# Kernel tuning notes

Measured on AMD Instinct MI355X. Metric: run time of the kernel, lower is better.

## Reference

```python
import jax, jax.numpy as jnp
import numpy as np

B, T, C = 2, 2048, 2048
NH, NKV = 16, 4
HD = C // NH  # 128


def setup_inputs() -> dict:
    key = jax.random.key(0)
    ks = jax.random.split(key, 5)
    w = lambda k, shape: jax.random.normal(k, shape, jnp.float32) * 0.02
    return {
        "x": jax.random.normal(ks[0], (B, T, C), jnp.float32),
        "Wq": w(ks[1], (C, C)),
        "Wk": w(ks[2], (C, NKV * HD)),
        "Wv": w(ks[3], (C, NKV * HD)),
        "Wproj": w(ks[4], (C, C)),
    }


def _rope(x):
    # x: [B, H, T, D]; rotate-half RoPE with base 10000
    D = x.shape[-1]
    t = x.shape[-2]
    inv_freq = 1.0 / (10000.0 ** (jnp.arange(0, D, 2, dtype=jnp.float32) / D))
    freqs = jnp.arange(t, dtype=jnp.float32)[:, None] * inv_freq[None, :]  # [T, D/2]
    emb = jnp.concatenate([freqs, freqs], axis=-1)  # [T, D]
    cos, sin = jnp.cos(emb), jnp.sin(emb)
    x1, x2 = x[..., : D // 2], x[..., D // 2 :]
    rotated = jnp.concatenate([-x2, x1], axis=-1)
    return x * cos + rotated * sin


def reference(x, Wq, Wk, Wv, Wproj):
    b, t, c = x.shape
    q = (x @ Wq).reshape(b, t, NH, HD).transpose(0, 2, 1, 3)    # [B,NH,T,HD]
    k = (x @ Wk).reshape(b, t, NKV, HD).transpose(0, 2, 1, 3)   # [B,NKV,T,HD]
    v = (x @ Wv).reshape(b, t, NKV, HD).transpose(0, 2, 1, 3)
    q = _rope(q)
    k = _rope(k)
    rep = NH // NKV
    k = jnp.repeat(k, rep, axis=1)  # [B,NH,T,HD]
    v = jnp.repeat(v, rep, axis=1)
    scale = 1.0 / jnp.sqrt(jnp.float32(HD))
    scores = jnp.einsum("bhqd,bhkd->bhqk", q, k) * scale        # [B,NH,T,T]
    causal = jnp.tril(jnp.ones((t, t), dtype=bool))
    scores = jnp.where(causal, scores, jnp.finfo(scores.dtype).min)
    attn = jax.nn.softmax(scores, axis=-1)
    y = jnp.einsum("bhqk,bhkd->bhqd", attn, v)                  # [B,NH,T,HD]
    y = y.transpose(0, 2, 1, 3).reshape(b, t, c)
    return y @ Wproj
```

## Files before the change

### kernel.cpp

```cpp
#include <hip/hip_runtime.h>

#define B_ 2
#define T_ 2048
#define C_ 2048
#define NH_ 16
#define NKV_ 4
#define HD_ 128
#define M_ 4096
#define NQKV_ 3072

typedef __bf16 bf16x8 __attribute__((ext_vector_type(8)));
typedef float f32x4 __attribute__((ext_vector_type(4)));
typedef float f32x16 __attribute__((ext_vector_type(16)));

__device__ __forceinline__ unsigned short f2bf(float f) {
  union { float f; unsigned u; } c{f};
  unsigned u = c.u + 0x7FFFu + ((c.u >> 16) & 1u);
  return (unsigned short)(u >> 16);
}
__device__ __forceinline__ float bf2f(unsigned short h) {
  union { unsigned u; float f; } c{(unsigned)h << 16};
  return c.f;
}

#define GLOAD_LDS16(g, l)                                        \
  __builtin_amdgcn_global_load_lds(                              \
      (const __attribute__((address_space(1))) void*)(g),        \
      (__attribute__((address_space(3))) void*)(l), 16, 0, 0)

__global__ void rope_table_kernel(float2* __restrict__ rt) {
  int t = blockIdx.x, i = threadIdx.x;
  float inv = powf(10000.f, -(float)(2 * i) / 128.f);
  float s, c;
  sincosf((float)t * inv, &s, &c);
  rt[t * 64 + i] = make_float2(c, s);
}

__global__ void convx_kernel(const float* __restrict__ x, unsigned short* __restrict__ xb, int n4) {
  int i = blockIdx.x * blockDim.x + threadIdx.x;
  if (i >= n4) return;
  float4 v = reinterpret_cast<const float4*>(x)[i];
  union { ushort4 u; unsigned short s[4]; } o;
  o.s[0] = f2bf(v.x); o.s[1] = f2bf(v.y); o.s[2] = f2bf(v.z); o.s[3] = f2bf(v.w);
  reinterpret_cast<ushort4*>(xb)[i] = o.u;
}

__global__ void transpose_conv4_kernel(const float* __restrict__ Wq, const float* __restrict__ Wk,
                                       const float* __restrict__ Wv, const float* __restrict__ Wp,
                                       unsigned short* __restrict__ wt) {
  __shared__ float tile[32][33];
  int id = blockIdx.x;
  const float* W;
  unsigned short* Wt;
  int N, bx, by;
  if (id < 4096)      { W = Wq; Wt = wt;                          N = 2048; int u = id;        bx = u & 63; by = u >> 6; }
  else if (id < 5120) { W = Wk; Wt = wt + (size_t)2048 * 2048;    N = 512;  int u = id - 4096; bx = u & 15; by = u >> 4; }
  else if (id < 6144) { W = Wv; Wt = wt + (size_t)2560 * 2048;    N = 512;  int u = id - 5120; bx = u & 15; by = u >> 4; }
  else                { W = Wp; Wt = wt + (size_t)3072 * 2048;    N = 2048; int u = id - 6144; bx = u & 63; by = u >> 6; }
  const int K = 2048;
  bx *= 32; by *= 32;
  int tx = threadIdx.x & 31, ty = threadIdx.x >> 5;
#pragma unroll
  for (int r = 0; r < 32; r += 8)
    tile[ty + r][tx] = W[(size_t)(by + ty + r) * N + bx + tx];
  __syncthreads();
#pragma unroll
  for (int r = 0; r < 32; r += 8)
    Wt[(size_t)(bx + ty + r) * K + by + tx] = f2bf(tile[tx][ty + r]);
}

__global__ void transpose_v_kernel(const unsigned short* __restrict__ qkv,
                                   unsigned short* __restrict__ vt2) {
  __shared__ unsigned short tile[64][136];
  int bt = blockIdx.x;
  int bh = bt >> 5, t = bt & 31;
  int b = bh >> 2, kvh = bh & 3;
  int tid = threadIdx.x;
#pragma unroll
  for (int p = 0; p < 4; ++p) {
    int kv = p * 16 + (tid >> 4);
    int c8 = (tid & 15) * 8;
    *reinterpret_cast<uint4*>(&tile[kv][c8]) = *reinterpret_cast<const uint4*>(
        &qkv[(size_t)(b * T_ + t * 64 + kv) * NQKV_ + 2560 + kvh * HD_ + c8]);
  }
  __syncthreads();
#pragma unroll
  for (int it = 0; it < 4; ++it) {
    int item = it * 256 + tid;
    int pk = item >> 7, d = item & 127;
    unsigned short tmp[8];
#pragma unroll
    for (int j = 0; j < 8; ++j) tmp[j] = tile[pk * 8 + j][d];
    *reinterpret_cast<uint4*>(&vt2[((size_t)(bt * 8 + pk) * 128 + d) * 8]) =
        *reinterpret_cast<uint4*>(tmp);
  }
}

template <typename OUT, bool ROPE>
__global__ __launch_bounds__(256) void gemm_bf16(const unsigned short* __restrict__ A,
                                                 const unsigned short* __restrict__ Bt,
                                                 OUT* __restrict__ Cm,
                                                 const float2* __restrict__ rt,
                                                 int M, int N, int K) {
  constexpr int BK = 32;
  __shared__ __align__(16) unsigned short Al[2][128 * BK];
  __shared__ __align__(16) unsigned short Bl[2][128 * BK];
  int tid = threadIdx.x, w = tid >> 6, lane = tid & 63;
  int l15 = lane & 15, l4 = lane >> 4;
  size_t arow0 = (size_t)blockIdx.y * 128;
  size_t brow0 = (size_t)blockIdx.x * 128;

  f32x4 acc[2][8];
#pragma unroll
  for (int mi = 0; mi < 2; ++mi)
#pragma unroll
    for (int ni = 0; ni < 8; ++ni) acc[mi][ni] = (f32x4){0.f, 0.f, 0.f, 0.f};

  auto stage = [&](int buf, int k0) {
#pragma unroll
    for (int i = 0; i < 2; ++i) {
      int c = i * 256 + w * 64 + lane;
      const unsigned short* g = A + (arow0 + (c >> 2)) * K + k0 + (c & 3) * 8;
      GLOAD_LDS16(g, &Al[buf][(i * 4 + w) * 512]);
    }
#pragma unroll
    for (int i = 0; i < 2; ++i) {
      int c = i * 256 + w * 64 + lane;
      const unsigned short* g = Bt + (brow0 + (c >> 2)) * K + k0 + (c & 3) * 8;
      GLOAD_LDS16(g, &Bl[buf][(i * 4 + w) * 512]);
    }
  };

  stage(0, 0);
  __syncthreads();
  int NT = K / BK, cur = 0;
  for (int kt = 0; kt < NT; ++kt) {
    if (kt + 1 < NT) stage(cur ^ 1, (kt + 1) * BK);
    const unsigned short* Ab = &Al[cur][0];
    const unsigned short* Bb = &Bl[cur][0];
    bf16x8 af[2], bfr[8];
#pragma unroll
    for (int mi = 0; mi < 2; ++mi)
      af[mi] = *reinterpret_cast<const bf16x8*>(Ab + (w * 32 + mi * 16 + l15) * BK + l4 * 8);
#pragma unroll
    for (int ni = 0; ni < 8; ++ni)
      bfr[ni] = *reinterpret_cast<const bf16x8*>(Bb + (ni * 16 + l15) * BK + l4 * 8);
#pragma unroll
    for (int mi = 0; mi < 2; ++mi)
#pragma unroll
      for (int ni = 0; ni < 8; ++ni)
        acc[mi][ni] = __builtin_amdgcn_mfma_f32_16x16x32_bf16(af[mi], bfr[ni], acc[mi][ni], 0, 0, 0);
    __syncthreads();
    cur ^= 1;
  }

  bool dorope = ROPE && (brow0 < 2560);
#pragma unroll
  for (int mi = 0; mi < 2; ++mi)
#pragma unroll
    for (int r = 0; r < 4; ++r) {
      size_t row = arow0 + w * 32 + mi * 16 + l4 * 4 + r;
      if (dorope) {
        int t = (int)(row & (T_ - 1));
#pragma unroll
        for (int ni = 0; ni < 4; ++ni) {
          float2 cs = rt[t * 64 + ni * 16 + l15];
          float a1 = acc[mi][ni][r], a2 = acc[mi][ni + 4][r];
          size_t col = brow0 + ni * 16 + l15;
          Cm[row * N + col]      = f2bf(a1 * cs.x - a2 * cs.y);
          Cm[row * N + col + 64] = f2bf(a2 * cs.x + a1 * cs.y);
        }
      } else {
#pragma unroll
        for (int ni = 0; ni < 8; ++ni) {
          size_t col = brow0 + ni * 16 + l15;
          float v = acc[mi][ni][r];
          if constexpr (sizeof(OUT) == 4) Cm[row * N + col] = v;
          else                            Cm[row * N + col] = f2bf(v);
        }
      }
    }
}

__global__ __launch_bounds__(256, 2) void attn_kernel(const unsigned short* __restrict__ qkv,
                                                      const unsigned short* __restrict__ vt2,
                                                      unsigned short* __restrict__ att) {
  constexpr int KB = 64;
  __shared__ __align__(16) unsigned short Kl[2][KB * 128];
  int tid = threadIdx.x, w = tid >> 6, lane = tid & 63;
  int l31 = lane & 31, hi = lane >> 5;
  int h4 = hi * 4;

  int id = blockIdx.x;
  int u = id & 255, half = id >> 8;
  int bh = u & 31;
  int qh = u >> 5;
  int qi = half ? (15 - qh) : qh;
  int q0 = qi * 128;
  int b = bh >> 4, hd = bh & 15, kvh = hd >> 2;
  int qr0 = q0 + w * 32;
  int ql = qr0 + l31;

  bf16x8 qf[8];
  {
    const unsigned short* qb = qkv + (size_t)(b * T_ + ql) * NQKV_ + hd * HD_ + hi * 8;
    const float scale = 0.08838834764831845f * 1.4426950408889634f;
#pragma unroll
    for (int df = 0; df < 8; ++df) {
      bf16x8 t = *reinterpret_cast<const bf16x8*>(qb + df * 16);
#pragma unroll
      for (int j = 0; j < 8; ++j) t[j] = (__bf16)((float)t[j] * scale);
      qf[df] = t;
    }
  }

  f32x16 o[4];
#pragma unroll
  for (int dt = 0; dt < 4; ++dt)
#pragma unroll
    for (int r = 0; r < 16; ++r) o[dt][r] = 0.f;
  float mr = -1e30f, lr = 0.f;

  auto stage_K = [&](int buf, int kv0) {
#pragma unroll
    for (int i = 0; i < 4; ++i) {
      int c = (i * 4 + w) * 64 + lane;
      int g = c ^ ((c >> 4) & 7);
      const unsigned short* src =
          qkv + (size_t)(b * T_ + kv0 + (g >> 4)) * NQKV_ + C_ + kvh * HD_ + (g & 15) * 8;
      GLOAD_LDS16(src, &Kl[buf][(i * 4 + w) * 512]);
    }
  };

  const unsigned short* vhead = vt2 + (size_t)((b * NKV_ + kvh) * 32) * 8192;

  int nt = q0 / KB + 2;
  stage_K(0, 0);
  __syncthreads();
  int cur = 0;
  for (int kt = 0; kt < nt; ++kt) {
    int kv0 = kt * KB;
    if (kt + 1 < nt) stage_K(cur ^ 1, kv0 + KB);

    if (kv0 <= qr0 + 31) {
      f32x16 s[2];
#pragma unroll
      for (int r = 0; r < 16; ++r) { s[0][r] = 0.f; s[1][r] = 0.f; }
      const unsigned short* Kb = &Kl[cur][0];
      __builtin_amdgcn_s_setprio(1);
#pragma unroll
      for (int t2 = 0; t2 < 2; ++t2)
#pragma unroll
        for (int df = 0; df < 8; ++df) {
          bf16x8 kf = *reinterpret_cast<const bf16x8*>(
              Kb + (((t2 * 32 + l31) * 128 + df * 16 + hi * 8) ^ ((l31 & 7) << 3)));
          s[t2] = __builtin_amdgcn_mfma_f32_32x32x16_bf16(kf, qf[df], s[t2], 0, 0, 0);
        }
      __builtin_amdgcn_s_setprio(0);

      float rm = -1e30f;
      if ((kv0 + KB - 1) > qr0) {
#pragma unroll
        for (int t2 = 0; t2 < 2; ++t2)
#pragma unroll
          for (int r = 0; r < 16; ++r) {
            float sv = s[t2][r];
            int kcol = kv0 + t2 * 32 + (r & 3) + 8 * (r >> 2) + h4;
            if (kcol > ql) sv = -1e30f;
            s[t2][r] = sv;
            rm = fmaxf(rm, sv);
          }
      } else {
#pragma unroll
        for (int t2 = 0; t2 < 2; ++t2)
#pragma unroll
          for (int r = 0; r < 16; ++r) rm = fmaxf(rm, s[t2][r]);
      }
      rm = fmaxf(rm, __shfl_xor(rm, 32));

      if (!__all(rm <= mr + 11.0f)) {
        float mnew = fmaxf(mr, rm);
        float alpha = exp2f(mr - mnew);
        mr = mnew;
        lr *= alpha;
#pragma unroll
        for (int dt = 0; dt < 4; ++dt)
#pragma unroll
          for (int r = 0; r < 16; ++r) o[dt][r] *= alpha;
      }

      float ps = 0.f;
#pragma unroll
      for (int t2 = 0; t2 < 2; ++t2)
#pragma unroll
        for (int r = 0; r < 16; ++r) {
          float p = exp2f(s[t2][r] - mr);
          s[t2][r] = p;
          ps += p;
        }
      lr += ps;

      unsigned pk[2][8];
#pragma unroll
      for (int t2 = 0; t2 < 2; ++t2)
#pragma unroll
        for (int i = 0; i < 8; ++i) {
          union { unsigned u32; __bf16 hh[2]; } pr;
          pr.hh[0] = (__bf16)s[t2][2 * i];
          pr.hh[1] = (__bf16)s[t2][2 * i + 1];
          pk[t2][i] = pr.u32;
        }

      const unsigned short* vb2 = vhead + (size_t)kt * 8192;
      uint4 va[4], vc[4];
#pragma unroll
      for (int kf = 0; kf < 4; ++kf)
        va[kf] = *reinterpret_cast<const uint4*>(vb2 + ((kf * 2 + hi) * 128 + l31) * 8);
#pragma unroll
      for (int kf = 0; kf < 4; ++kf)
        vc[kf] = *reinterpret_cast<const uint4*>(vb2 + ((kf * 2 + hi) * 128 + 32 + l31) * 8);

      bf16x8 pb[4];
#pragma unroll
      for (int f = 0; f < 4; ++f) {
        int t2 = f >> 1, bq = (f & 1) * 4;
        union { bf16x8 v; unsigned d[4]; } fr;
#pragma unroll
        for (int p = 0; p < 2; ++p) {
          unsigned a = pk[t2][bq + p];
          unsigned bb = pk[t2][bq + 2 + p];
          asm("v_permlane32_swap_b32 %0, %1" : "+v"(a), "+v"(bb));
          fr.d[p] = a;
          fr.d[2 + p] = bb;
        }
        pb[f] = fr.v;
      }

      union Vc { uint4 u; bf16x8 v; };
      __builtin_amdgcn_s_setprio(1);
#pragma unroll
      for (int kf = 0; kf < 4; ++kf) {
        Vc cv; cv.u = va[kf];
        o[0] = __builtin_amdgcn_mfma_f32_32x32x16_bf16(cv.v, pb[kf], o[0], 0, 0, 0);
      }
#pragma unroll
      for (int kf = 0; kf < 4; ++kf)
        va[kf] = *reinterpret_cast<const uint4*>(vb2 + ((kf * 2 + hi) * 128 + 64 + l31) * 8);
#pragma unroll
      for (int kf = 0; kf < 4; ++kf) {
        Vc cv; cv.u = vc[kf];
        o[1] = __builtin_amdgcn_mfma_f32_32x32x16_bf16(cv.v, pb[kf], o[1], 0, 0, 0);
      }
#pragma unroll
      for (int kf = 0; kf < 4; ++kf)
        vc[kf] = *reinterpret_cast<const uint4*>(vb2 + ((kf * 2 + hi) * 128 + 96 + l31) * 8);
#pragma unroll
      for (int kf = 0; kf < 4; ++kf) {
        Vc cv; cv.u = va[kf];
        o[2] = __builtin_amdgcn_mfma_f32_32x32x16_bf16(cv.v, pb[kf], o[2], 0, 0, 0);
      }
#pragma unroll
      for (int kf = 0; kf < 4; ++kf) {
        Vc cv; cv.u = vc[kf];
        o[3] = __builtin_amdgcn_mfma_f32_32x32x16_bf16(cv.v, pb[kf], o[3], 0, 0, 0);
      }
      __builtin_amdgcn_s_setprio(0);
    }

    __syncthreads();
    cur ^= 1;
  }

  float ls = lr + __shfl_xor(lr, 32);
  float inv = 1.f / ls;
  unsigned short* ob = att + (size_t)(b * T_ + ql) * C_ + hd * HD_;
#pragma unroll
  for (int dt = 0; dt < 4; ++dt)
#pragma unroll
    for (int r = 0; r < 16; ++r) {
      int d = dt * 32 + (r & 3) + 8 * (r >> 2) + h4;
      ob[d] = f2bf(o[dt][r] * inv);
    }
}

extern "C" void kernel_launch(void* const* d_in, const int* in_sizes, int n_in,
                              void* d_out, int out_size, void* d_ws, size_t ws_size,
                              hipStream_t stream) {
  const float* x  = (const float*)d_in[0];
  const float* Wq = (const float*)d_in[1];
  const float* Wk = (const float*)d_in[2];
  const float* Wv = (const float*)d_in[3];
  const float* Wp = (const float*)d_in[4];
  float* out = (float*)d_out;
  char* ws = (char*)d_ws;

  unsigned short* xb  = (unsigned short*)(ws);
  unsigned short* wt  = (unsigned short*)(ws + 16777216);
  unsigned short* qkv = (unsigned short*)(ws + 37748736);
  float2*         rt  = (float2*)(ws + 62914560);
  unsigned short* vt  = (unsigned short*)(ws + 63963136);
  unsigned short* att = xb;

  rope_table_kernel<<<T_, 64, 0, stream>>>(rt);
  convx_kernel<<<(M_ * C_ / 4 + 255) / 256, 256, 0, stream>>>(x, xb, M_ * C_ / 4);
  transpose_conv4_kernel<<<dim3(10240), 256, 0, stream>>>(Wq, Wk, Wv, Wp, wt);

  gemm_bf16<unsigned short, true><<<dim3(NQKV_ / 128, M_ / 128), 256, 0, stream>>>(
      xb, wt, qkv, rt, M_, NQKV_, C_);
  transpose_v_kernel<<<dim3(256), 256, 0, stream>>>(qkv, vt);
  attn_kernel<<<dim3(512), 256, 0, stream>>>(qkv, vt, att);
  gemm_bf16<float, false><<<dim3(C_ / 128, M_ / 128), 256, 0, stream>>>(
      att, wt + (size_t)3072 * 2048, out, nullptr, M_, C_, C_);
}
```

Measured before the change: 222.5 us.

## Write K/V pre-tiled from QKV GEMM epilogue; single-wave attention reading global directly

The QKV GEMM epilogue now writes Q, RoPE-rotated K, and V directly into per-tile blocked layouts, which removes the separate V transpose kernel. The attention kernel becomes a one-wave block over 32 query rows and fetches K fragments straight from global memory, dropping LDS staging and block barriers. It also gets finer causal work granularity across 2048 blocks. In exchange, K/V reuse across waves no longer happens in LDS, so K/V global/L2 traffic rises, and the epilogue's scattered 2-byte stores may be less coalesced.

Measured after the change: 272.6 us. 22.5% more time.

```diff
diff --git a/kernel.cpp b/kernel.cpp
--- a/kernel.cpp
+++ b/kernel.cpp
@@ -17,10 +17,6 @@
   union { float f; unsigned u; } c{f};
   unsigned u = c.u + 0x7FFFu + ((c.u >> 16) & 1u);
   return (unsigned short)(u >> 16);
-}
-__device__ __forceinline__ float bf2f(unsigned short h) {
-  union { unsigned u; float f; } c{(unsigned)h << 16};
-  return c.f;
 }
 
 #define GLOAD_LDS16(g, l)                                        \
@@ -69,37 +65,13 @@
     Wt[(size_t)(bx + ty + r) * K + by + tx] = f2bf(tile[tx][ty + r]);
 }
 
-__global__ void transpose_v_kernel(const unsigned short* __restrict__ qkv,
-                                   unsigned short* __restrict__ vt2) {
-  __shared__ unsigned short tile[64][136];
-  int bt = blockIdx.x;
-  int bh = bt >> 5, t = bt & 31;
-  int b = bh >> 2, kvh = bh & 3;
-  int tid = threadIdx.x;
-#pragma unroll
-  for (int p = 0; p < 4; ++p) {
-    int kv = p * 16 + (tid >> 4);
-    int c8 = (tid & 15) * 8;
-    *reinterpret_cast<uint4*>(&tile[kv][c8]) = *reinterpret_cast<const uint4*>(
-        &qkv[(size_t)(b * T_ + t * 64 + kv) * NQKV_ + 2560 + kvh * HD_ + c8]);
-  }
-  __syncthreads();
-#pragma unroll
-  for (int it = 0; it < 4; ++it) {
-    int item = it * 256 + tid;
-    int pk = item >> 7, d = item & 127;
-    unsigned short tmp[8];
-#pragma unroll
-    for (int j = 0; j < 8; ++j) tmp[j] = tile[pk * 8 + j][d];
-    *reinterpret_cast<uint4*>(&vt2[((size_t)(bt * 8 + pk) * 128 + d) * 8]) =
-        *reinterpret_cast<uint4*>(tmp);
-  }
-}
-
-template <typename OUT, bool ROPE>
+template <int MODE>
 __global__ __launch_bounds__(256) void gemm_bf16(const unsigned short* __restrict__ A,
                                                  const unsigned short* __restrict__ Bt,
-                                                 OUT* __restrict__ Cm,
+                                                 float* __restrict__ Cout,
+                                                 unsigned short* __restrict__ qb,
+                                                 unsigned short* __restrict__ kt2,
+                                                 unsigned short* __restrict__ vt2,
                                                  const float2* __restrict__ rt,
                                                  int M, int N, int K) {
   constexpr int BK = 32;
@@ -154,60 +126,80 @@
     cur ^= 1;
   }
 
-  bool dorope = ROPE && (brow0 < 2560);
-#pragma unroll
-  for (int mi = 0; mi < 2; ++mi)
-#pragma unroll
-    for (int r = 0; r < 4; ++r) {
-      size_t row = arow0 + w * 32 + mi * 16 + l4 * 4 + r;
-      if (dorope) {
-        int t = (int)(row & (T_ - 1));
-#pragma unroll
-        for (int ni = 0; ni < 4; ++ni) {
-          float2 cs = rt[t * 64 + ni * 16 + l15];
-          float a1 = acc[mi][ni][r], a2 = acc[mi][ni + 4][r];
-          size_t col = brow0 + ni * 16 + l15;
-          Cm[row * N + col]      = f2bf(a1 * cs.x - a2 * cs.y);
-          Cm[row * N + col + 64] = f2bf(a2 * cs.x + a1 * cs.y);
-        }
-      } else {
-#pragma unroll
-        for (int ni = 0; ni < 8; ++ni) {
-          size_t col = brow0 + ni * 16 + l15;
-          float v = acc[mi][ni][r];
-          if constexpr (sizeof(OUT) == 4) Cm[row * N + col] = v;
-          else                            Cm[row * N + col] = f2bf(v);
+  if constexpr (MODE == 0) {
+#pragma unroll
+    for (int mi = 0; mi < 2; ++mi)
+#pragma unroll
+      for (int r = 0; r < 4; ++r) {
+        size_t row = arow0 + w * 32 + mi * 16 + l4 * 4 + r;
+#pragma unroll
+        for (int ni = 0; ni < 8; ++ni)
+          Cout[row * N + brow0 + ni * 16 + l15] = acc[mi][ni][r];
+      }
+  } else {
+    bool isq = brow0 < 2048;
+    bool isk = !isq && brow0 < 2560;
+    int kvh = isq ? 0 : (int)((brow0 - (isk ? 2048 : 2560)) >> 7);
+#pragma unroll
+    for (int mi = 0; mi < 2; ++mi)
+#pragma unroll
+      for (int r = 0; r < 4; ++r) {
+        size_t row = arow0 + w * 32 + mi * 16 + l4 * 4 + r;
+        int bb = (int)(row >> 11), t = (int)(row & 2047);
+        if (isq) {
+#pragma unroll
+          for (int ni = 0; ni < 4; ++ni) {
+            float2 cs = rt[t * 64 + ni * 16 + l15];
+            float a1 = acc[mi][ni][r], a2 = acc[mi][ni + 4][r];
+            size_t col = brow0 + ni * 16 + l15;
+            qb[row * 2048 + col]      = f2bf(a1 * cs.x - a2 * cs.y);
+            qb[row * 2048 + col + 64] = f2bf(a2 * cs.x + a1 * cs.y);
+          }
+        } else if (isk) {
+          int tile = t >> 6, kv = t & 63;
+          size_t base = (size_t)((bb * 4 + kvh) * 32 + tile) * 8192;
+#pragma unroll
+          for (int ni = 0; ni < 4; ++ni) {
+            int d = ni * 16 + l15;
+            float2 cs = rt[t * 64 + d];
+            float a1 = acc[mi][ni][r], a2 = acc[mi][ni + 4][r];
+            int d2 = d + 64;
+            kt2[base + (size_t)(d >> 3) * 512 + kv * 8 + (d & 7)]   = f2bf(a1 * cs.x - a2 * cs.y);
+            kt2[base + (size_t)(d2 >> 3) * 512 + kv * 8 + (d2 & 7)] = f2bf(a2 * cs.x + a1 * cs.y);
+          }
+        } else {
+          int tile = t >> 6, kv = t & 63;
+          size_t base = (size_t)((bb * 4 + kvh) * 32 + tile) * 8192;
+#pragma unroll
+          for (int ni = 0; ni < 8; ++ni) {
+            int d = ni * 16 + l15;
+            vt2[base + (size_t)(kv >> 3) * 1024 + d * 8 + (kv & 7)] = f2bf(acc[mi][ni][r]);
+          }
         }
       }
-    }
-}
-
-__global__ __launch_bounds__(256, 2) void attn_kernel(const unsigned short* __restrict__ qkv,
-                                                      const unsigned short* __restrict__ vt2,
-                                                      unsigned short* __restrict__ att) {
-  constexpr int KB = 64;
-  __shared__ __align__(16) unsigned short Kl[2][KB * 128];
-  int tid = threadIdx.x, w = tid >> 6, lane = tid & 63;
-  int l31 = lane & 31, hi = lane >> 5;
-  int h4 = hi * 4;
-
+  }
+}
+
+__global__ __launch_bounds__(64) void attn_kernel(const unsigned short* __restrict__ qb,
+                                                  const unsigned short* __restrict__ kt2,
+                                                  const unsigned short* __restrict__ vt2,
+                                                  unsigned short* __restrict__ att) {
+  int lane = threadIdx.x, l31 = lane & 31, hi = lane >> 5, h4 = hi * 4;
   int id = blockIdx.x;
-  int u = id & 255, half = id >> 8;
-  int bh = u & 31;
-  int qh = u >> 5;
-  int qi = half ? (15 - qh) : qh;
-  int q0 = qi * 128;
+  int u = id & 1023, half = id >> 10;
+  int bh = u & 31, qq = u >> 5;
+  int qi = half ? (63 - qq) : qq;
+  int q0 = qi * 32;
   int b = bh >> 4, hd = bh & 15, kvh = hd >> 2;
-  int qr0 = q0 + w * 32;
-  int ql = qr0 + l31;
+  int ql = q0 + l31;
 
   bf16x8 qf[8];
   {
-    const unsigned short* qb = qkv + (size_t)(b * T_ + ql) * NQKV_ + hd * HD_ + hi * 8;
+    const unsigned short* qp = qb + (size_t)(b * T_ + ql) * 2048 + hd * HD_ + hi * 8;
     const float scale = 0.08838834764831845f * 1.4426950408889634f;
 #pragma unroll
     for (int df = 0; df < 8; ++df) {
-      bf16x8 t = *reinterpret_cast<const bf16x8*>(qb + df * 16);
+      bf16x8 t = *reinterpret_cast<const bf16x8*>(qp + df * 16);
 #pragma unroll
       for (int j = 0; j < 8; ++j) t[j] = (__bf16)((float)t[j] * scale);
       qf[df] = t;
@@ -221,154 +213,160 @@
     for (int r = 0; r < 16; ++r) o[dt][r] = 0.f;
   float mr = -1e30f, lr = 0.f;
 
-  auto stage_K = [&](int buf, int kv0) {
-#pragma unroll
-    for (int i = 0; i < 4; ++i) {
-      int c = (i * 4 + w) * 64 + lane;
-      int g = c ^ ((c >> 4) & 7);
-      const unsigned short* src =
-          qkv + (size_t)(b * T_ + kv0 + (g >> 4)) * NQKV_ + C_ + kvh * HD_ + (g & 15) * 8;
-      GLOAD_LDS16(src, &Kl[buf][(i * 4 + w) * 512]);
-    }
-  };
-
-  const unsigned short* vhead = vt2 + (size_t)((b * NKV_ + kvh) * 32) * 8192;
-
-  int nt = q0 / KB + 2;
-  stage_K(0, 0);
-  __syncthreads();
-  int cur = 0;
+  int nt = (qi >> 1) + 1;
+  const unsigned short* kb = kt2 + (size_t)((b * 4 + kvh) * 32) * 8192;
+  const unsigned short* vb = vt2 + (size_t)((b * 4 + kvh) * 32) * 8192;
+
+  union Vc { uint4 u; bf16x8 v; };
   for (int kt = 0; kt < nt; ++kt) {
-    int kv0 = kt * KB;
-    if (kt + 1 < nt) stage_K(cur ^ 1, kv0 + KB);
-
-    if (kv0 <= qr0 + 31) {
-      f32x16 s[2];
-#pragma unroll
-      for (int r = 0; r < 16; ++r) { s[0][r] = 0.f; s[1][r] = 0.f; }
-      const unsigned short* Kb = &Kl[cur][0];
-      __builtin_amdgcn_s_setprio(1);
+    int kv0 = kt * 64;
+    const unsigned short* kbt = kb + (size_t)kt * 8192;
+    const unsigned short* vbt = vb + (size_t)kt * 8192;
+
+    f32x16 s[2];
+#pragma unroll
+    for (int r = 0; r < 16; ++r) { s[0][r] = 0.f; s[1][r] = 0.f; }
+    uint4 kx[4], ky[4];
+#pragma unroll
+    for (int df = 0; df < 4; ++df)
+      kx[df] = *reinterpret_cast<const uint4*>(kbt + ((df * 2 + hi) * 64 + l31) * 8);
+#pragma unroll
+    for (int df = 0; df < 4; ++df)
+      ky[df] = *reinterpret_cast<const uint4*>(kbt + (((df + 4) * 2 + hi) * 64 + l31) * 8);
+    __builtin_amdgcn_s_setprio(1);
+#pragma unroll
+    for (int df = 0; df < 4; ++df) {
+      Vc c; c.u = kx[df];
+      s[0] = __builtin_amdgcn_mfma_f32_32x32x16_bf16(c.v, qf[df], s[0], 0, 0, 0);
+    }
+#pragma unroll
+    for (int df = 0; df < 4; ++df)
+      kx[df] = *reinterpret_cast<const uint4*>(kbt + ((df * 2 + hi) * 64 + 32 + l31) * 8);
+#pragma unroll
+    for (int df = 0; df < 4; ++df) {
+      Vc c; c.u = ky[df];
+      s[0] = __builtin_amdgcn_mfma_f32_32x32x16_bf16(c.v, qf[df + 4], s[0], 0, 0, 0);
+    }
+#pragma unroll
+    for (int df = 0; df < 4; ++df)
+      ky[df] = *reinterpret_cast<const uint4*>(kbt + (((df + 4) * 2 + hi) * 64 + 32 + l31) * 8);
+#pragma unroll
+    for (int df = 0; df < 4; ++df) {
+      Vc c; c.u = kx[df];
+      s[1] = __builtin_amdgcn_mfma_f32_32x32x16_bf16(c.v, qf[df], s[1], 0, 0, 0);
+    }
+#pragma unroll
+    for (int df = 0; df < 4; ++df) {
+      Vc c; c.u = ky[df];
+      s[1] = __builtin_amdgcn_mfma_f32_32x32x16_bf16(c.v, qf[df + 4], s[1], 0, 0, 0);
+    }
+    __builtin_amdgcn_s_setprio(0);
+
+    float rm = -1e30f;
+    if (kv0 + 63 > q0) {
 #pragma unroll
       for (int t2 = 0; t2 < 2; ++t2)
 #pragma unroll
-        for (int df = 0; df < 8; ++df) {
-          bf16x8 kf = *reinterpret_cast<const bf16x8*>(
-              Kb + (((t2 * 32 + l31) * 128 + df * 16 + hi * 8) ^ ((l31 & 7) << 3)));
-          s[t2] = __builtin_amdgcn_mfma_f32_32x32x16_bf16(kf, qf[df], s[t2], 0, 0, 0);
+        for (int r = 0; r < 16; ++r) {
+          float sv = s[t2][r];
+          int kcol = kv0 + t2 * 32 + (r & 3) + 8 * (r >> 2) + h4;
+          if (kcol > ql) sv = -1e30f;
+          s[t2][r] = sv;
+          rm = fmaxf(rm, sv);
         }
-      __builtin_amdgcn_s_setprio(0);
-
-      float rm = -1e30f;
-      if ((kv0 + KB - 1) > qr0) {
-#pragma unroll
-        for (int t2 = 0; t2 < 2; ++t2)
-#pragma unroll
-          for (int r = 0; r < 16; ++r) {
-            float sv = s[t2][r];
-            int kcol = kv0 + t2 * 32 + (r & 3) + 8 * (r >> 2) + h4;
-            if (kcol > ql) sv = -1e30f;
-            s[t2][r] = sv;
-            rm = fmaxf(rm, sv);
-          }
-      } else {
-#pragma unroll
-        for (int t2 = 0; t2 < 2; ++t2)
-#pragma unroll
-          for (int r = 0; r < 16; ++r) rm = fmaxf(rm, s[t2][r]);
+    } else {
+#pragma unroll
+      for (int t2 = 0; t2 < 2; ++t2)
+#pragma unroll
+        for (int r = 0; r < 16; ++r) rm = fmaxf(rm, s[t2][r]);
+    }
+    rm = fmaxf(rm, __shfl_xor(rm, 32));
+
+    if (!__all(rm <= mr + 11.0f)) {
+      float mnew = fmaxf(mr, rm);
+      float alpha = exp2f(mr - mnew);
+      mr = mnew;
+      lr *= alpha;
+#pragma unroll
+      for (int dt = 0; dt < 4; ++dt)
+#pragma unroll
+        for (int r = 0; r < 16; ++r) o[dt][r] *= alpha;
+    }
+
+    float ps = 0.f;
+#pragma unroll
+    for (int t2 = 0; t2 < 2; ++t2)
+#pragma unroll
+      for (int r = 0; r < 16; ++r) {
+        float p = exp2f(s[t2][r] - mr);
+        s[t2][r] = p;
+        ps += p;
       }
-      rm = fmaxf(rm, __shfl_xor(rm, 32));
-
-      if (!__all(rm <= mr + 11.0f)) {
-        float mnew = fmaxf(mr, rm);
-        float alpha = exp2f(mr - mnew);
-        mr = mnew;
-        lr *= alpha;
-#pragma unroll
-        for (int dt = 0; dt < 4; ++dt)
-#pragma unroll
-          for (int r = 0; r < 16; ++r) o[dt][r] *= alpha;
+    lr += ps;
+
+    unsigned pk[2][8];
+#pragma unroll
+    for (int t2 = 0; t2 < 2; ++t2)
+#pragma unroll
+      for (int i = 0; i < 8; ++i) {
+        union { unsigned u32; __bf16 hh[2]; } pr;
+        pr.hh[0] = (__bf16)s[t2][2 * i];
+        pr.hh[1] = (__bf16)s[t2][2 * i + 1];
+        pk[t2][i] = pr.u32;
       }
 
-      float ps = 0.f;
-#pragma unroll
-      for (int t2 = 0; t2 < 2; ++t2)
-#pragma unroll
-        for (int r = 0; r < 16; ++r) {
-          float p = exp2f(s[t2][r] - mr);
-          s[t2][r] = p;
-          ps += p;
-        }
-      lr += ps;
-
-      unsigned pk[2][8];
-#pragma unroll
-      for (int t2 = 0; t2 < 2; ++t2)
-#pragma unroll
-        for (int i = 0; i < 8; ++i) {
-          union { unsigned u32; __bf16 hh[2]; } pr;
-          pr.hh[0] = (__bf16)s[t2][2 * i];
-          pr.hh[1] = (__bf16)s[t2][2 * i + 1];
-          pk[t2][i] = pr.u32;
-        }
-
-      const unsigned short* vb2 = vhead + (size_t)kt * 8192;
-      uint4 va[4], vc[4];
-#pragma unroll
-      for (int kf = 0; kf < 4; ++kf)
-        va[kf] = *reinterpret_cast<const uint4*>(vb2 + ((kf * 2 + hi) * 128 + l31) * 8);
-#pragma unroll
-      for (int kf = 0; kf < 4; ++kf)
-        vc[kf] = *reinterpret_cast<const uint4*>(vb2 + ((kf * 2 + hi) * 128 + 32 + l31) * 8);
-
-      bf16x8 pb[4];
-#pragma unroll
-      for (int f = 0; f < 4; ++f) {
-        int t2 = f >> 1, bq = (f & 1) * 4;
-        union { bf16x8 v; unsigned d[4]; } fr;
-#pragma unroll
-        for (int p = 0; p < 2; ++p) {
-          unsigned a = pk[t2][bq + p];
-          unsigned bb = pk[t2][bq + 2 + p];
-          asm("v_permlane32_swap_b32 %0, %1" : "+v"(a), "+v"(bb));
-          fr.d[p] = a;
-          fr.d[2 + p] = bb;
-        }
-        pb[f] = fr.v;
+    uint4 va[4], vc[4];
+#pragma unroll
+    for (int kf = 0; kf < 4; ++kf)
+      va[kf] = *reinterpret_cast<const uint4*>(vbt + ((kf * 2 + hi) * 128 + l31) * 8);
+#pragma unroll
+    for (int kf = 0; kf < 4; ++kf)
+      vc[kf] = *reinterpret_cast<const uint4*>(vbt + ((kf * 2 + hi) * 128 + 32 + l31) * 8);
+
+    bf16x8 pb[4];
+#pragma unroll
+    for (int f = 0; f < 4; ++f) {
+      int t2 = f >> 1, bq = (f & 1) * 4;
+      union { bf16x8 v; unsigned d[4]; } fr;
+#pragma unroll
+      for (int p = 0; p < 2; ++p) {
+        unsigned a = pk[t2][bq + p];
+        unsigned bb2 = pk[t2][bq + 2 + p];
+        asm("v_permlane32_swap_b32 %0, %1" : "+v"(a), "+v"(bb2));
+        fr.d[p] = a;
+        fr.d[2 + p] = bb2;
       }
-
-      union Vc { uint4 u; bf16x8 v; };
-      __builtin_amdgcn_s_setprio(1);
-#pragma unroll
-      for (int kf = 0; kf < 4; ++kf) {
-        Vc cv; cv.u = va[kf];
-        o[0] = __builtin_amdgcn_mfma_f32_32x32x16_bf16(cv.v, pb[kf], o[0], 0, 0, 0);
-      }
-#pragma unroll
-      for (int kf = 0; kf < 4; ++kf)
-        va[kf] = *reinterpret_cast<const uint4*>(vb2 + ((kf * 2 + hi) * 128 + 64 + l31) * 8);
-#pragma unroll
-      for (int kf = 0; kf < 4; ++kf) {
-        Vc cv; cv.u = vc[kf];
-        o[1] = __builtin_amdgcn_mfma_f32_32x32x16_bf16(cv.v, pb[kf], o[1], 0, 0, 0);
-      }
-#pragma unroll
-      for (int kf = 0; kf < 4; ++kf)
-        vc[kf] = *reinterpret_cast<const uint4*>(vb2 + ((kf * 2 + hi) * 128 + 96 + l31) * 8);
-#pragma unroll
-      for (int kf = 0; kf < 4; ++kf) {
-        Vc cv; cv.u = va[kf];
-        o[2] = __builtin_amdgcn_mfma_f32_32x32x16_bf16(cv.v, pb[kf], o[2], 0, 0, 0);
-      }
-#pragma unroll
-      for (int kf = 0; kf < 4; ++kf) {
-        Vc cv; cv.u = vc[kf];
-        o[3] = __builtin_amdgcn_mfma_f32_32x32x16_bf16(cv.v, pb[kf], o[3], 0, 0, 0);
-      }
-      __builtin_amdgcn_s_setprio(0);
-    }
-
-    __syncthreads();
-    cur ^= 1;
+      pb[f] = fr.v;
+    }
+
+    __builtin_amdgcn_s_setprio(1);
+#pragma unroll
+    for (int kf = 0; kf < 4; ++kf) {
+      Vc c; c.u = va[kf];
+      o[0] = __builtin_amdgcn_mfma_f32_32x32x16_bf16(c.v, pb[kf], o[0], 0, 0, 0);
+    }
+#pragma unroll
+    for (int kf = 0; kf < 4; ++kf)
+      va[kf] = *reinterpret_cast<const uint4*>(vbt + ((kf * 2 + hi) * 128 + 64 + l31) * 8);
+#pragma unroll
+    for (int kf = 0; kf < 4; ++kf) {
+      Vc c; c.u = vc[kf];
+      o[1] = __builtin_amdgcn_mfma_f32_32x32x16_bf16(c.v, pb[kf], o[1], 0, 0, 0);
+    }
+#pragma unroll
+    for (int kf = 0; kf < 4; ++kf)
+      vc[kf] = *reinterpret_cast<const uint4*>(vbt + ((kf * 2 + hi) * 128 + 96 + l31) * 8);
+#pragma unroll
+    for (int kf = 0; kf < 4; ++kf) {
+      Vc c; c.u = va[kf];
+      o[2] = __builtin_amdgcn_mfma_f32_32x32x16_bf16(c.v, pb[kf], o[2], 0, 0, 0);
+    }
+#pragma unroll
+    for (int kf = 0; kf < 4; ++kf) {
+      Vc c; c.u = vc[kf];
+      o[3] = __builtin_amdgcn_mfma_f32_32x32x16_bf16(c.v, pb[kf], o[3], 0, 0, 0);
+    }
+    __builtin_amdgcn_s_setprio(0);
   }
 
   float ls = lr + __shfl_xor(lr, 32);
@@ -396,19 +394,19 @@
 
   unsigned short* xb  = (unsigned short*)(ws);
   unsigned short* wt  = (unsigned short*)(ws + 16777216);
-  unsigned short* qkv = (unsigned short*)(ws + 37748736);
-  float2*         rt  = (float2*)(ws + 62914560);
-  unsigned short* vt  = (unsigned short*)(ws + 63963136);
+  unsigned short* qb  = (unsigned short*)(ws + 37748736);
+  float2*         rt  = (float2*)(ws + 54525952);
+  unsigned short* kt2 = (unsigned short*)(ws + 55574528);
+  unsigned short* vt2 = (unsigned short*)(ws + 59768832);
   unsigned short* att = xb;
 
   rope_table_kernel<<<T_, 64, 0, stream>>>(rt);
   convx_kernel<<<(M_ * C_ / 4 + 255) / 256, 256, 0, stream>>>(x, xb, M_ * C_ / 4);
   transpose_conv4_kernel<<<dim3(10240), 256, 0, stream>>>(Wq, Wk, Wv, Wp, wt);
 
-  gemm_bf16<unsigned short, true><<<dim3(NQKV_ / 128, M_ / 128), 256, 0, stream>>>(
-      xb, wt, qkv, rt, M_, NQKV_, C_);
-  transpose_v_kernel<<<dim3(256), 256, 0, stream>>>(qkv, vt);
-  attn_kernel<<<dim3(512), 256, 0, stream>>>(qkv, vt, att);
-  gemm_bf16<float, false><<<dim3(C_ / 128, M_ / 128), 256, 0, stream>>>(
-      att, wt + (size_t)3072 * 2048, out, nullptr, M_, C_, C_);
-}
+  gemm_bf16<1><<<dim3(NQKV_ / 128, M_ / 128), 256, 0, stream>>>(
+      xb, wt, nullptr, qb, kt2, vt2, rt, M_, NQKV_, C_);
+  attn_kernel<<<dim3(2048), 64, 0, stream>>>(qb, kt2, vt2, att);
+  gemm_bf16<0><<<dim3(C_ / 128, M_ / 128), 256, 0, stream>>>(
+      att, wt + (size_t)3072 * 2048, out, nullptr, nullptr, nullptr, nullptr, M_, C_, C_);
+}
```

## Split attention into single-wave blocks of 32 query rows without K double-buffering

Applied to the files above, without the earlier changes.

The attention kernel now launches 2048 one-wave blocks, each owning 32 query rows, instead of 512 four-wave blocks covering 128 rows that shared a double-buffered K tile in LDS. Each wave loads its own 64-row K tile into a single LDS buffer and waits on vmcnt(0) before computing, so barriers and the fully masked tail iterations go away. The aim is finer-grained causal load balancing and more independent blocks for the scheduler. In exchange, K reuse across waves is lost, which raises global and L2 traffic, and K loads no longer overlap with compute.

Result: slower. 241.4 us (+8.5%).

```diff
diff --git a/kernel.cpp b/kernel.cpp
--- a/kernel.cpp
+++ b/kernel.cpp
@@ -17,10 +17,6 @@
   union { float f; unsigned u; } c{f};
   unsigned u = c.u + 0x7FFFu + ((c.u >> 16) & 1u);
   return (unsigned short)(u >> 16);
-}
-__device__ __forceinline__ float bf2f(unsigned short h) {
-  union { unsigned u; float f; } c{(unsigned)h << 16};
-  return c.f;
 }
 
 #define GLOAD_LDS16(g, l)                                        \
@@ -182,32 +178,26 @@
     }
 }
 
-__global__ __launch_bounds__(256, 2) void attn_kernel(const unsigned short* __restrict__ qkv,
-                                                      const unsigned short* __restrict__ vt2,
-                                                      unsigned short* __restrict__ att) {
-  constexpr int KB = 64;
-  __shared__ __align__(16) unsigned short Kl[2][KB * 128];
-  int tid = threadIdx.x, w = tid >> 6, lane = tid & 63;
-  int l31 = lane & 31, hi = lane >> 5;
-  int h4 = hi * 4;
-
+__global__ __launch_bounds__(64) void attn_kernel(const unsigned short* __restrict__ qkv,
+                                                  const unsigned short* __restrict__ vt2,
+                                                  unsigned short* __restrict__ att) {
+  __shared__ __align__(16) unsigned short Kl[64 * 128];
+  int lane = threadIdx.x, l31 = lane & 31, hi = lane >> 5, h4 = hi * 4;
   int id = blockIdx.x;
-  int u = id & 255, half = id >> 8;
-  int bh = u & 31;
-  int qh = u >> 5;
-  int qi = half ? (15 - qh) : qh;
-  int q0 = qi * 128;
+  int u = id & 1023, half = id >> 10;
+  int bh = u & 31, qq = u >> 5;
+  int qi = half ? (63 - qq) : qq;
+  int q0 = qi * 32;
   int b = bh >> 4, hd = bh & 15, kvh = hd >> 2;
-  int qr0 = q0 + w * 32;
-  int ql = qr0 + l31;
+  int ql = q0 + l31;
 
   bf16x8 qf[8];
   {
-    const unsigned short* qb = qkv + (size_t)(b * T_ + ql) * NQKV_ + hd * HD_ + hi * 8;
+    const unsigned short* qp = qkv + (size_t)(b * T_ + ql) * NQKV_ + hd * HD_ + hi * 8;
     const float scale = 0.08838834764831845f * 1.4426950408889634f;
 #pragma unroll
     for (int df = 0; df < 8; ++df) {
-      bf16x8 t = *reinterpret_cast<const bf16x8*>(qb + df * 16);
+      bf16x8 t = *reinterpret_cast<const bf16x8*>(qp + df * 16);
 #pragma unroll
       for (int j = 0; j < 8; ++j) t[j] = (__bf16)((float)t[j] * scale);
       qf[df] = t;
@@ -221,154 +211,143 @@
     for (int r = 0; r < 16; ++r) o[dt][r] = 0.f;
   float mr = -1e30f, lr = 0.f;
 
-  auto stage_K = [&](int buf, int kv0) {
-#pragma unroll
-    for (int i = 0; i < 4; ++i) {
-      int c = (i * 4 + w) * 64 + lane;
+  int nt = (qi >> 1) + 1;
+  const unsigned short* vb = vt2 + (size_t)((b * 4 + kvh) * 32) * 8192;
+
+  union Vc { uint4 u; bf16x8 v; };
+  for (int kt = 0; kt < nt; ++kt) {
+    int kv0 = kt * 64;
+
+#pragma unroll
+    for (int i = 0; i < 16; ++i) {
+      int c = i * 64 + lane;
       int g = c ^ ((c >> 4) & 7);
       const unsigned short* src =
           qkv + (size_t)(b * T_ + kv0 + (g >> 4)) * NQKV_ + C_ + kvh * HD_ + (g & 15) * 8;
-      GLOAD_LDS16(src, &Kl[buf][(i * 4 + w) * 512]);
-    }
-  };
-
-  const unsigned short* vhead = vt2 + (size_t)((b * NKV_ + kvh) * 32) * 8192;
-
-  int nt = q0 / KB + 2;
-  stage_K(0, 0);
-  __syncthreads();
-  int cur = 0;
-  for (int kt = 0; kt < nt; ++kt) {
-    int kv0 = kt * KB;
-    if (kt + 1 < nt) stage_K(cur ^ 1, kv0 + KB);
-
-    if (kv0 <= qr0 + 31) {
-      f32x16 s[2];
-#pragma unroll
-      for (int r = 0; r < 16; ++r) { s[0][r] = 0.f; s[1][r] = 0.f; }
-      const unsigned short* Kb = &Kl[cur][0];
-      __builtin_amdgcn_s_setprio(1);
+      GLOAD_LDS16(src, &Kl[i * 512]);
+    }
+    asm volatile("s_waitcnt vmcnt(0)" ::: "memory");
+
+    f32x16 s[2];
+#pragma unroll
+    for (int r = 0; r < 16; ++r) { s[0][r] = 0.f; s[1][r] = 0.f; }
+    __builtin_amdgcn_s_setprio(1);
+#pragma unroll
+    for (int t2 = 0; t2 < 2; ++t2)
+#pragma unroll
+      for (int df = 0; df < 8; ++df) {
+        bf16x8 kf = *reinterpret_cast<const bf16x8*>(
+            Kl + (((t2 * 32 + l31) * 128 + df * 16 + hi * 8) ^ ((l31 & 7) << 3)));
+        s[t2] = __builtin_amdgcn_mfma_f32_32x32x16_bf16(kf, qf[df], s[t2], 0, 0, 0);
+      }
+    __builtin_amdgcn_s_setprio(0);
+
+    float rm = -1e30f;
+    if (kv0 + 63 > q0) {
 #pragma unroll
       for (int t2 = 0; t2 < 2; ++t2)
 #pragma unroll
-        for (int df = 0; df < 8; ++df) {
-          bf16x8 kf = *reinterpret_cast<const bf16x8*>(
-              Kb + (((t2 * 32 + l31) * 128 + df * 16 + hi * 8) ^ ((l31 & 7) << 3)));
-          s[t2] = __builtin_amdgcn_mfma_f32_32x32x16_bf16(kf, qf[df], s[t2], 0, 0, 0);
+        for (int r = 0; r < 16; ++r) {
+          float sv = s[t2][r];
+          int kcol = kv0 + t2 * 32 + (r & 3) + 8 * (r >> 2) + h4;
+          if (kcol > ql) sv = -1e30f;
+          s[t2][r] = sv;
+          rm = fmaxf(rm, sv);
         }
-      __builtin_amdgcn_s_setprio(0);
-
-      float rm = -1e30f;
-      if ((kv0 + KB - 1) > qr0) {
-#pragma unroll
-        for (int t2 = 0; t2 < 2; ++t2)
-#pragma unroll
-          for (int r = 0; r < 16; ++r) {
-            float sv = s[t2][r];
-            int kcol = kv0 + t2 * 32 + (r & 3) + 8 * (r >> 2) + h4;
-            if (kcol > ql) sv = -1e30f;
-            s[t2][r] = sv;
-            rm = fmaxf(rm, sv);
-          }
-      } else {
-#pragma unroll
-        for (int t2 = 0; t2 < 2; ++t2)
-#pragma unroll
-          for (int r = 0; r < 16; ++r) rm = fmaxf(rm, s[t2][r]);
-      }
-      rm = fmaxf(rm, __shfl_xor(rm, 32));
-
-      if (!__all(rm <= mr + 11.0f)) {
-        float mnew = fmaxf(mr, rm);
-        float alpha = exp2f(mr - mnew);
-        mr = mnew;
-        lr *= alpha;
-#pragma unroll
-        for (int dt = 0; dt < 4; ++dt)
-#pragma unroll
-          for (int r = 0; r < 16; ++r) o[dt][r] *= alpha;
-      }
-
-      float ps = 0.f;
+    } else {
 #pragma unroll
       for (int t2 = 0; t2 < 2; ++t2)
 #pragma unroll
-        for (int r = 0; r < 16; ++r) {
-          float p = exp2f(s[t2][r] - mr);
-          s[t2][r] = p;
-          ps += p;
-        }
-      lr += ps;
-
-      unsigned pk[2][8];
-#pragma unroll
-      for (int t2 = 0; t2 < 2; ++t2)
-#pragma unroll
-        for (int i = 0; i < 8; ++i) {
-          union { unsigned u32; __bf16 hh[2]; } pr;
-          pr.hh[0] = (__bf16)s[t2][2 * i];
-          pr.hh[1] = (__bf16)s[t2][2 * i + 1];
-          pk[t2][i] = pr.u32;
-        }
-
-      const unsigned short* vb2 = vhead + (size_t)kt * 8192;
-      uint4 va[4], vc[4];
-#pragma unroll
-      for (int kf = 0; kf < 4; ++kf)
-        va[kf] = *reinterpret_cast<const uint4*>(vb2 + ((kf * 2 + hi) * 128 + l31) * 8);
-#pragma unroll
-      for (int kf = 0; kf < 4; ++kf)
-        vc[kf] = *reinterpret_cast<const uint4*>(vb2 + ((kf * 2 + hi) * 128 + 32 + l31) * 8);
-
-      bf16x8 pb[4];
-#pragma unroll
-      for (int f = 0; f < 4; ++f) {
-        int t2 = f >> 1, bq = (f & 1) * 4;
-        union { bf16x8 v; unsigned d[4]; } fr;
-#pragma unroll
-        for (int p = 0; p < 2; ++p) {
-          unsigned a = pk[t2][bq + p];
-          unsigned bb = pk[t2][bq + 2 + p];
-          asm("v_permlane32_swap_b32 %0, %1" : "+v"(a), "+v"(bb));
-          fr.d[p] = a;
-          fr.d[2 + p] = bb;
-        }
-        pb[f] = fr.v;
-      }
-
-      union Vc { uint4 u; bf16x8 v; };
-      __builtin_amdgcn_s_setprio(1);
-#pragma unroll
-      for (int kf = 0; kf < 4; ++kf) {
-        Vc cv; cv.u = va[kf];
-        o[0] = __builtin_amdgcn_mfma_f32_32x32x16_bf16(cv.v, pb[kf], o[0], 0, 0, 0);
-      }
-#pragma unroll
-      for (int kf = 0; kf < 4; ++kf)
-        va[kf] = *reinterpret_cast<const uint4*>(vb2 + ((kf * 2 + hi) * 128 + 64 + l31) * 8);
-#pragma unroll
-      for (int kf = 0; kf < 4; ++kf) {
-        Vc cv; cv.u = vc[kf];
-        o[1] = __builtin_amdgcn_mfma_f32_32x32x16_bf16(cv.v, pb[kf], o[1], 0, 0, 0);
-      }
-#pragma unroll
-      for (int kf = 0; kf < 4; ++kf)
-        vc[kf] = *reinterpret_cast<const uint4*>(vb2 + ((kf * 2 + hi) * 128 + 96 + l31) * 8);
-#pragma unroll
-      for (int kf = 0; kf < 4; ++kf) {
-        Vc cv; cv.u = va[kf];
-        o[2] = __builtin_amdgcn_mfma_f32_32x32x16_bf16(cv.v, pb[kf], o[2], 0, 0, 0);
-      }
-#pragma unroll
-      for (int kf = 0; kf < 4; ++kf) {
-        Vc cv; cv.u = vc[kf];
-        o[3] = __builtin_amdgcn_mfma_f32_32x32x16_bf16(cv.v, pb[kf], o[3], 0, 0, 0);
-      }
-      __builtin_amdgcn_s_setprio(0);
-    }
-
-    __syncthreads();
-    cur ^= 1;
+        for (int r = 0; r < 16; ++r) rm = fmaxf(rm, s[t2][r]);
+    }
+    rm = fmaxf(rm, __shfl_xor(rm, 32));
+
+    if (!__all(rm <= mr + 11.0f)) {
+      float mnew = fmaxf(mr, rm);
+      float alpha = exp2f(mr - mnew);
+      mr = mnew;
+      lr *= alpha;
+#pragma unroll
+      for (int dt = 0; dt < 4; ++dt)
+#pragma unroll
+        for (int r = 0; r < 16; ++r) o[dt][r] *= alpha;
+    }
+
+    float ps = 0.f;
+#pragma unroll
+    for (int t2 = 0; t2 < 2; ++t2)
+#pragma unroll
+      for (int r = 0; r < 16; ++r) {
+        float p = exp2f(s[t2][r] - mr);
+        s[t2][r] = p;
+        ps += p;
+      }
+    lr += ps;
+
+    unsigned pk[2][8];
+#pragma unroll
+    for (int t2 = 0; t2 < 2; ++t2)
+#pragma unroll
+      for (int i = 0; i < 8; ++i) {
+        union { unsigned u32; __bf16 hh[2]; } pr;
+        pr.hh[0] = (__bf16)s[t2][2 * i];
+        pr.hh[1] = (__bf16)s[t2][2 * i + 1];
+        pk[t2][i] = pr.u32;
+      }
+
+    const unsigned short* vbt = vb + (size_t)kt * 8192;
+    uint4 va[4], vc[4];
+#pragma unroll
+    for (int kf = 0; kf < 4; ++kf)
+      va[kf] = *reinterpret_cast<const uint4*>(vbt + ((kf * 2 + hi) * 128 + l31) * 8);
+#pragma unroll
+    for (int kf = 0; kf < 4; ++kf)
+      vc[kf] = *reinterpret_cast<const uint4*>(vbt + ((kf * 2 + hi) * 128 + 32 + l31) * 8);
+
+    bf16x8 pb[4];
+#pragma unroll
+    for (int f = 0; f < 4; ++f) {
+      int t2 = f >> 1, bq = (f & 1) * 4;
+      union { bf16x8 v; unsigned d[4]; } fr;
+#pragma unroll
+      for (int p = 0; p < 2; ++p) {
+        unsigned a = pk[t2][bq + p];
+        unsigned bb2 = pk[t2][bq + 2 + p];
+        asm("v_permlane32_swap_b32 %0, %1" : "+v"(a), "+v"(bb2));
+        fr.d[p] = a;
+        fr.d[2 + p] = bb2;
+      }
+      pb[f] = fr.v;
+    }
+
+    __builtin_amdgcn_s_setprio(1);
+#pragma unroll
+    for (int kf = 0; kf < 4; ++kf) {
+      Vc c; c.u = va[kf];
+      o[0] = __builtin_amdgcn_mfma_f32_32x32x16_bf16(c.v, pb[kf], o[0], 0, 0, 0);
+    }
+#pragma unroll
+    for (int kf = 0; kf < 4; ++kf)
+      va[kf] = *reinterpret_cast<const uint4*>(vbt + ((kf * 2 + hi) * 128 + 64 + l31) * 8);
+#pragma unroll
+    for (int kf = 0; kf < 4; ++kf) {
+      Vc c; c.u = vc[kf];
+      o[1] = __builtin_amdgcn_mfma_f32_32x32x16_bf16(c.v, pb[kf], o[1], 0, 0, 0);
+    }
+#pragma unroll
+    for (int kf = 0; kf < 4; ++kf)
+      vc[kf] = *reinterpret_cast<const uint4*>(vbt + ((kf * 2 + hi) * 128 + 96 + l31) * 8);
+#pragma unroll
+    for (int kf = 0; kf < 4; ++kf) {
+      Vc c; c.u = va[kf];
+      o[2] = __builtin_amdgcn_mfma_f32_32x32x16_bf16(c.v, pb[kf], o[2], 0, 0, 0);
+    }
+#pragma unroll
+    for (int kf = 0; kf < 4; ++kf) {
+      Vc c; c.u = vc[kf];
+      o[3] = __builtin_amdgcn_mfma_f32_32x32x16_bf16(c.v, pb[kf], o[3], 0, 0, 0);
+    }
+    __builtin_amdgcn_s_setprio(0);
   }
 
   float ls = lr + __shfl_xor(lr, 32);
@@ -398,7 +377,7 @@
   unsigned short* wt  = (unsigned short*)(ws + 16777216);
   unsigned short* qkv = (unsigned short*)(ws + 37748736);
   float2*         rt  = (float2*)(ws + 62914560);
-  unsigned short* vt  = (unsigned short*)(ws + 63963136);
+  unsigned short* vt2 = (unsigned short*)(ws + 63963136);
   unsigned short* att = xb;
 
   rope_table_kernel<<<T_, 64, 0, stream>>>(rt);
@@ -407,8 +386,8 @@
 
   gemm_bf16<unsigned short, true><<<dim3(NQKV_ / 128, M_ / 128), 256, 0, stream>>>(
       xb, wt, qkv, rt, M_, NQKV_, C_);
-  transpose_v_kernel<<<dim3(256), 256, 0, stream>>>(qkv, vt);
-  attn_kernel<<<dim3(512), 256, 0, stream>>>(qkv, vt, att);
+  transpose_v_kernel<<<dim3(256), 256, 0, stream>>>(qkv, vt2);
+  attn_kernel<<<dim3(2048), 64, 0, stream>>>(qkv, vt2, att);
   gemm_bf16<float, false><<<dim3(C_ / 128, M_ / 128), 256, 0, stream>>>(
       att, wt + (size_t)3072 * 2048, out, nullptr, M_, C_, C_);
 }
```
